# Kernel tuning notes

Hardware: AMD Instinct MI355X
Metric: run time of the kernel (lower is better)

## Reference

```python
import jax, jax.numpy as jnp
import numpy as np

N = 10000      # nodes
E = 65536      # edges
IN = 16        # in_channels
H = 64         # hidden_channels
ED = 4         # edge_attr_dim
MLP_H = 64     # hidden width of edge-weight MLPs


def _glorot(key, shape):
    fan_in, fan_out = shape[0], shape[1]
    lim = np.sqrt(6.0 / (fan_in + fan_out)).astype(np.float32)
    return jax.random.uniform(key, shape, jnp.float32, -lim, lim)


def setup_inputs() -> dict:
    key = jax.random.key(0)
    ks = jax.random.split(key, 16)
    x = jax.random.normal(ks[0], (N, IN), dtype=jnp.float32)
    edge_index = jax.random.randint(ks[1], (2, E), 0, N, dtype=jnp.int64)
    edge_attr = jax.random.normal(ks[2], (E, ED), dtype=jnp.float32)
    return {
        "x": x,
        "edge_index": edge_index,
        "edge_attr": edge_attr,
        # nn1: Linear(ED,64) -> ReLU -> Linear(64, IN*H)
        "nn1_w1": _glorot(ks[3], (ED, MLP_H)), "nn1_b1": jnp.zeros((MLP_H,), jnp.float32),
        "nn1_w2": _glorot(ks[4], (MLP_H, IN * H)), "nn1_b2": jnp.zeros((IN * H,), jnp.float32),
        "root1": _glorot(ks[5], (IN, H)), "bias1": jnp.zeros((H,), jnp.float32),
        # nn2: Linear(ED,64) -> ReLU -> Linear(64, H*H)
        "nn2_w1": _glorot(ks[6], (ED, MLP_H)), "nn2_b1": jnp.zeros((MLP_H,), jnp.float32),
        "nn2_w2": _glorot(ks[7], (MLP_H, H * H)), "nn2_b2": jnp.zeros((H * H,), jnp.float32),
        "root2": _glorot(ks[8], (H, H)), "bias2": jnp.zeros((H,), jnp.float32),
        # readout MLP
        "lin1_w": _glorot(ks[9], (H, 8)), "lin1_b": jnp.zeros((8,), jnp.float32),
        "lin2_w": _glorot(ks[10], (8, 1)), "lin2_b": jnp.zeros((1,), jnp.float32),
    }


def _nnconv(x, src, dst, edge_attr, w1, b1, w2, b2, root, bias, cin, cout):
    # Edge-conditioned weight generation: MLP(edge_attr) -> [E, cin, cout]
    h = jax.nn.relu(edge_attr @ w1 + b1)
    We = (h @ w2 + b2).reshape(-1, cin, cout)
    # Per-edge matmul: message_e = x[src_e] @ We_e  -> [E, cout]
    msg = jnp.einsum('ei,eio->eo', x[src], We)
    # Scatter mean over destination nodes
    s = jax.ops.segment_sum(msg, dst, num_segments=N)
    cnt = jax.ops.segment_sum(jnp.ones((msg.shape[0],), x.dtype), dst, num_segments=N)
    agg = s / jnp.maximum(cnt, 1.0)[:, None]
    # Root transform + bias (PyG NNConv defaults: root_weight=True, bias=True)
    return agg + x @ root + bias


def reference(x, edge_index, edge_attr,
              nn1_w1, nn1_b1, nn1_w2, nn1_b2, root1, bias1,
              nn2_w1, nn2_b1, nn2_w2, nn2_b2, root2, bias2,
              lin1_w, lin1_b, lin2_w, lin2_b):
    # Dropout layers are identity in eval mode.
    src, dst = edge_index[0], edge_index[1]
    h = jax.nn.relu(_nnconv(x, src, dst, edge_attr,
                            nn1_w1, nn1_b1, nn1_w2, nn1_b2, root1, bias1, IN, H))
    h = jax.nn.relu(_nnconv(h, src, dst, edge_attr,
                            nn2_w1, nn2_b1, nn2_w2, nn2_b2, root2, bias2, H, H))
    h = jax.nn.relu(h @ lin1_w + lin1_b)
    return (h @ lin2_w + lin2_b)[:, 0]  # squeeze(-1) -> [N]
```

## Files before the change

### kernel.cpp

```cpp
#include <hip/hip_runtime.h>
#include <hip/hip_bf16.h>

#define NN 10000
#define EE 65536

using short8  = __attribute__((ext_vector_type(8))) short;
using u16x8   = __attribute__((ext_vector_type(8))) unsigned short;
using float4v = __attribute__((ext_vector_type(4))) float;

__device__ __forceinline__ unsigned short f2b(float f){
  union { float f; unsigned int u; } v; v.f = f;
  unsigned int u = v.u;
  unsigned int r = (u + 0x7fff + ((u >> 16) & 1)) >> 16;
  return (unsigned short)r;
}

__device__ __forceinline__ short8 ntload(const unsigned short* p){
  return __builtin_nontemporal_load((const short8*)p);
}



__device__ __forceinline__ void do_permB(int idx, const float* __restrict__ w2,
                                         unsigned short* __restrict__ Bt,
                                         int cin, int s , int cb ){
  int tile   = idx >> 9;
  int within = idx & 511;
  int ot  = tile >> s;
  int k32 = tile & ((1<<s)-1);
  int kk   = within & 31;
  int orow = within >> 5;
  int o = ot*16 + orow;
  int k = k32*32 + kk;
  int m = k >> cb;
  int i = k & (cin-1);
  Bt[idx] = f2b(w2[(size_t)m*(cin*64) + i*64 + o]);
}

__global__ __launch_bounds__(256) void k_prep(
    const float* __restrict__ w2a, unsigned short* __restrict__ Bt1,
    const float* __restrict__ w2b, unsigned short* __restrict__ Bt2,
    int* __restrict__ cnt){
  int b = blockIdx.x;
  int t = threadIdx.x;
  if(b < 40){
    int i = b*256 + t;
    if(i < NN) cnt[i] = 0;
  } else if(b < 296){
    do_permB((b-40)*256 + t, w2a, Bt1, 16, 5, 4);
  } else {
    do_permB((b-296)*256 + t, w2b, Bt2, 64, 7, 6);
  }
}


__global__ void k_hist(const int* __restrict__ dst, int* __restrict__ cnt){
  int e = blockIdx.x*256 + threadIdx.x;
  if(e < EE) atomicAdd(&cnt[dst[e]], 1);
}

__global__ __launch_bounds__(1024) void k_scan(const int* __restrict__ cnt, int* __restrict__ offs, int* __restrict__ cursor){
  const int T = 1024, PER = (NN + T - 1)/T;
  int tid = threadIdx.x;
  int base = tid*PER;
  int local[PER];
  int s = 0;
  #pragma unroll
  for(int j=0;j<PER;j++){
    int i = base+j;
    int v = (i<NN)? cnt[i] : 0;
    local[j] = s;
    s += v;
  }
  int lane = tid & 63, wv = tid >> 6;
  int val = s;
  #pragma unroll
  for(int o=1;o<64;o<<=1){
    int u = __shfl_up(val, o, 64);
    if(lane >= o) val += u;
  }
  __shared__ int wsum[16];
  if(lane==63) wsum[wv] = val;
  __syncthreads();
  if(tid==0){
    int acc=0;
    #pragma unroll
    for(int i=0;i<16;i++){ int t2=wsum[i]; wsum[i]=acc; acc+=t2; }
  }
  __syncthreads();
  int thr_excl = wsum[wv] + (val - s);
  #pragma unroll
  for(int j=0;j<PER;j++){
    int i = base+j;
    if(i<NN){ int e = thr_excl + local[j]; offs[i]=e; cursor[i]=e; }
  }
  if(tid == T-1) offs[NN] = thr_excl + s;
}

__global__ void k_scatter(const int* __restrict__ dst, const int* __restrict__ src,
                          int* __restrict__ cursor, int2* __restrict__ elist2){
  int e = blockIdx.x*256 + threadIdx.x;
  if(e < EE){ int p = atomicAdd(&cursor[dst[e]], 1); elist2[p] = make_int2(e, src[e]); }
}


__global__ __launch_bounds__(64) void k_accK1(const float* __restrict__ x,
    const int* __restrict__ offs, const int2* __restrict__ elist2,
    const float* __restrict__ ea, const float* __restrict__ w1, const float* __restrict__ b1,
    unsigned short* __restrict__ K1, float* __restrict__ XS, int v0){
  int v = v0 + blockIdx.x;
  int L = threadIdx.x;
  int cg = L & 3, mg = L >> 2;
  int i0 = cg << 2;
  float w1c0 = w1[L], w1c1 = w1[64+L], w1c2 = w1[128+L], w1c3 = w1[192+L];
  float b1c = b1[L];
  __shared__ float sh[2][64];
  float acc[4][4];
  #pragma unroll
  for(int j=0;j<4;j++)
    #pragma unroll
    for(int c=0;c<4;c++) acc[j][c]=0.f;
  float4 xs = make_float4(0.f,0.f,0.f,0.f);
  int p0 = offs[v], p1 = offs[v+1];
  float4 a_nxt = make_float4(0.f,0.f,0.f,0.f);
  float4 x_nxt = make_float4(0.f,0.f,0.f,0.f);
  if(p0 < p1){
    int2 es = elist2[p0];
    a_nxt = *(const float4*)(ea + (size_t)es.x*4);
    x_nxt = *(const float4*)(x + (size_t)es.y*16 + i0);
  }
  for(int p=p0;p<p1;p++){
    int buf = (p-p0)&1;
    float4 xv = x_nxt;
    float4 av = a_nxt;
    float hv = fmaxf(b1c + av.x*w1c0 + av.y*w1c1 + av.z*w1c2 + av.w*w1c3, 0.f);
    sh[buf][L] = hv;
    __syncthreads();
    if(p+1<p1){
      int2 es = elist2[p+1];
      a_nxt = *(const float4*)(ea + (size_t)es.x*4);
      x_nxt = *(const float4*)(x + (size_t)es.y*16 + i0);
    }
    xs.x += xv.x; xs.y += xv.y; xs.z += xv.z; xs.w += xv.w;
    #pragma unroll
    for(int j=0;j<4;j++){
      float hm = sh[buf][mg + 16*j];
      acc[j][0] += hm*xv.x; acc[j][1] += hm*xv.y;
      acc[j][2] += hm*xv.z; acc[j][3] += hm*xv.w;
    }
  }
  int r = blockIdx.x;
  int rt = r >> 4, lrow = r & 15;
  #pragma unroll
  for(int j=0;j<4;j++){
    int m = mg + 16*j;
    size_t sidx = ((size_t)(rt*32 + (m>>1)))*512
                + (size_t)lrow*32 + (m&1)*16 + cg*4;
    ushort4 u;
    u.x=f2b(acc[j][0]); u.y=f2b(acc[j][1]); u.z=f2b(acc[j][2]); u.w=f2b(acc[j][3]);
    *(ushort4*)(K1 + sidx) = u;
  }
  if(mg==0) *(float4*)(XS + (size_t)v*64 + i0) = xs;
}


__global__ __launch_bounds__(64) void k_accK2(const float* __restrict__ x1,
    const int* __restrict__ offs, const int2* __restrict__ elist2,
    const float* __restrict__ ea, const float* __restrict__ w1, const float* __restrict__ b1,
    unsigned short* __restrict__ K, float* __restrict__ XS, int v0){
  int v = v0 + blockIdx.x;
  int L = threadIdx.x;
  int cg = L & 7, mg = L >> 3;
  int i0 = cg << 3;
  float w1c0 = w1[L], w1c1 = w1[64+L], w1c2 = w1[128+L], w1c3 = w1[192+L];
  float b1c = b1[L];
  __shared__ float sh[2][64];
  float acc[8][8];
  #pragma unroll
  for(int j=0;j<8;j++)
    #pragma unroll
    for(int c=0;c<8;c++) acc[j][c]=0.f;
  float4 xs0 = make_float4(0.f,0.f,0.f,0.f);
  float4 xs1 = make_float4(0.f,0.f,0.f,0.f);
  int p0 = offs[v], p1 = offs[v+1];
  float4 a_nxt = make_float4(0.f,0.f,0.f,0.f);
  float4 x_nxt0 = make_float4(0.f,0.f,0.f,0.f);
  float4 x_nxt1 = make_float4(0.f,0.f,0.f,0.f);
  if(p0 < p1){
    int2 es = elist2[p0];
    a_nxt = *(const float4*)(ea + (size_t)es.x*4);
    const float* xr = x1 + (size_t)es.y*64 + i0;
    x_nxt0 = *(const float4*)xr;
    x_nxt1 = *(const float4*)(xr+4);
  }
  for(int p=p0;p<p1;p++){
    int buf = (p-p0)&1;
    float4 xv0 = x_nxt0, xv1 = x_nxt1;
    float4 av = a_nxt;
    float hv = fmaxf(b1c + av.x*w1c0 + av.y*w1c1 + av.z*w1c2 + av.w*w1c3, 0.f);
    sh[buf][L] = hv;
    __syncthreads();
    if(p+1<p1){
      int2 es = elist2[p+1];
      a_nxt = *(const float4*)(ea + (size_t)es.x*4);
      const float* xr = x1 + (size_t)es.y*64 + i0;
      x_nxt0 = *(const float4*)xr;
      x_nxt1 = *(const float4*)(xr+4);
    }
    xs0.x += xv0.x; xs0.y += xv0.y; xs0.z += xv0.z; xs0.w += xv0.w;
    xs1.x += xv1.x; xs1.y += xv1.y; xs1.z += xv1.z; xs1.w += xv1.w;
    float4 h4a = *(float4*)&sh[buf][mg*8];
    float4 h4b = *(float4*)&sh[buf][mg*8+4];
    #pragma unroll
    for(int jj=0;jj<2;jj++){
      float4 h4 = jj? h4b : h4a;
      #pragma unroll
      for(int tq=0;tq<4;tq++){
        int j = jj*4+tq;
        float hm = (tq==0)?h4.x:(tq==1)?h4.y:(tq==2)?h4.z:h4.w;
        acc[j][0] += hm*xv0.x; acc[j][1] += hm*xv0.y;
        acc[j][2] += hm*xv0.z; acc[j][3] += hm*xv0.w;
        acc[j][4] += hm*xv1.x; acc[j][5] += hm*xv1.y;
        acc[j][6] += hm*xv1.z; acc[j][7] += hm*xv1.w;
      }
    }
  }
  int r = blockIdx.x;
  int rt = r >> 4, lrow = r & 15;
  #pragma unroll
  for(int j=0;j<8;j++){
    int m = mg*8 + j;
    size_t sidx = ((size_t)(rt*128 + m*2 + (cg>>2)))*512
                + (size_t)lrow*32 + (cg&3)*8;
    u16x8 u;
    #pragma unroll
    for(int c=0;c<8;c++) u[c] = f2b(acc[j][c]);
    *(u16x8*)(K + sidx) = u;
  }
  if(mg==0){
    *(float4*)(XS + (size_t)v*64 + i0)     = xs0;
    *(float4*)(XS + (size_t)v*64 + i0 + 4) = xs1;
  }
}


template<int KT32, int TSTEPS>
__global__ __launch_bounds__(512) void k_gemmS(const unsigned short* __restrict__ A,
    const unsigned short* __restrict__ Bt, float* __restrict__ P,
    int ntiles, int rowsChunk){
  __shared__ unsigned short Bs[4*TSTEPS*512];
  int tid = threadIdx.x;
  int lane = tid & 63;
  int w = tid >> 6;
  int s = blockIdx.y;
  int kbase = s*TSTEPS;

  constexpr int NT = 4*TSTEPS;
  constexpr int PERW = NT/8;
  #pragma unroll
  for(int it=0; it<PERW; it++){
    int g = w*PERW + it;
    int ct = g / TSTEPS, t = g - ct*TSTEPS;
    *(short8*)(Bs + (size_t)g*512 + lane*8) =
        *(const short8*)(Bt + (((size_t)ct*KT32 + kbase + t) << 9) + lane*8);
  }
  __syncthreads();

  int lrt = blockIdx.x*8 + w;
  if(lrt >= ntiles) return;

  int lperm = (lane & 15)*32 + (lane >> 4)*8;
  const unsigned short* Ap = A + (((size_t)lrt*KT32 + kbase) << 9) + lperm;
  const unsigned short* BsL = Bs + lperm;

  float4v acc0{}, acc1{}, acc2{}, acc3{};
  short8 ab[4];
  #pragma unroll
  for(int t=0;t<4;t++) ab[t] = ntload(Ap + t*512);

  #pragma unroll
  for(int t=0;t<TSTEPS;t++){
    short8 a  = ab[t&3];
    short8 b0 = *(const short8*)(BsL + (0*TSTEPS+t)*512);
    short8 b1 = *(const short8*)(BsL + (1*TSTEPS+t)*512);
    short8 b2 = *(const short8*)(BsL + (2*TSTEPS+t)*512);
    short8 b3 = *(const short8*)(BsL + (3*TSTEPS+t)*512);
    acc0 = __builtin_amdgcn_mfma_f32_16x16x32_bf16(a, b0, acc0, 0,0,0);
    acc1 = __builtin_amdgcn_mfma_f32_16x16x32_bf16(a, b1, acc1, 0,0,0);
    acc2 = __builtin_amdgcn_mfma_f32_16x16x32_bf16(a, b2, acc2, 0,0,0);
    acc3 = __builtin_amdgcn_mfma_f32_16x16x32_bf16(a, b3, acc3, 0,0,0);
    if(t+4 < TSTEPS) ab[t&3] = ntload(Ap + (t+4)*512);
  }

  int lrow = lane & 15, quad = lane >> 4;
  float* Pr = P + ((size_t)s*rowsChunk + lrt*16 + quad*4)*64 + lrow;
  #pragma unroll
  for(int reg=0;reg<4;reg++){
    Pr[(size_t)reg*64 +  0] = acc0[reg];
    Pr[(size_t)reg*64 + 16] = acc1[reg];
    Pr[(size_t)reg*64 + 32] = acc2[reg];
    Pr[(size_t)reg*64 + 48] = acc3[reg];
  }
}


template<int CIN, int SPLIT>
__global__ __launch_bounds__(256) void k_reduce_ep(const float* __restrict__ P, int rows, int v0,
    const float* __restrict__ XS, const float* __restrict__ b2, const float* __restrict__ xprev,
    const float* __restrict__ root, const float* __restrict__ bias, const int* __restrict__ offs,
    float* __restrict__ out){
  int idx = blockIdx.x*256 + threadIdx.x;
  if(idx >= rows*16) return;
  int r = idx >> 4, og = (idx & 15) << 2;
  int v = v0 + r;

  float4 s = make_float4(0.f,0.f,0.f,0.f);
  #pragma unroll
  for(int z=0; z<SPLIT; z++){
    float4 p = *(const float4*)(P + ((size_t)z*rows + r)*64 + og);
    s.x += p.x; s.y += p.y; s.z += p.z; s.w += p.w;
  }
  #pragma unroll
  for(int i=0;i<CIN;i++){
    float xsv = XS[(size_t)v*64 + i];
    float4 b = *(const float4*)(b2 + i*64 + og);
    s.x += xsv*b.x; s.y += xsv*b.y; s.z += xsv*b.z; s.w += xsv*b.w;
  }
  float4 rt = make_float4(0.f,0.f,0.f,0.f);
  #pragma unroll
  for(int i=0;i<CIN;i++){
    float xv = xprev[(size_t)v*CIN + i];
    float4 wv = *(const float4*)(root + i*64 + og);
    rt.x += xv*wv.x; rt.y += xv*wv.y; rt.z += xv*wv.z; rt.w += xv*wv.w;
  }
  float c = (float)(offs[v+1]-offs[v]); c = fmaxf(c, 1.f);
  float inv = 1.f/c;
  float4 bi = *(const float4*)(bias + og);
  float4 o;
  o.x = fmaxf(s.x*inv + rt.x + bi.x, 0.f);
  o.y = fmaxf(s.y*inv + rt.y + bi.y, 0.f);
  o.z = fmaxf(s.z*inv + rt.z + bi.z, 0.f);
  o.w = fmaxf(s.w*inv + rt.w + bi.w, 0.f);
  *(float4*)(out + (size_t)v*64 + og) = o;
}


template<int SPLIT>
__global__ __launch_bounds__(256) void k_red2_ro(const float* __restrict__ P, int rows, int v0,
    const float* __restrict__ XS, const float* __restrict__ b2, const float* __restrict__ x1,
    const float* __restrict__ root, const float* __restrict__ bias, const int* __restrict__ offs,
    const float* __restrict__ lw1, const float* __restrict__ lb1,
    const float* __restrict__ lw2, const float* __restrict__ lb2,
    float* __restrict__ out){
  __shared__ float row[16][68];
  __shared__ float hjs[16][8];
  int tid = threadIdx.x;
  int idx = blockIdx.x*256 + tid;
  int r = idx >> 4, og = (idx & 15) << 2;
  int n = tid >> 4;
  int nbase = blockIdx.x*16;
  int ninblk = rows - nbase; if(ninblk > 16) ninblk = 16;

  float4 o = make_float4(0.f,0.f,0.f,0.f);
  if(r < rows){
    int vg = v0 + r;
    float4 s = make_float4(0.f,0.f,0.f,0.f);
    #pragma unroll
    for(int z=0; z<SPLIT; z++){
      float4 p = *(const float4*)(P + ((size_t)z*rows + r)*64 + og);
      s.x += p.x; s.y += p.y; s.z += p.z; s.w += p.w;
    }
    #pragma unroll
    for(int i=0;i<64;i++){
      float xsv = XS[(size_t)vg*64 + i];
      float4 b = *(const float4*)(b2 + i*64 + og);
      s.x += xsv*b.x; s.y += xsv*b.y; s.z += xsv*b.z; s.w += xsv*b.w;
    }
    float4 rt = make_float4(0.f,0.f,0.f,0.f);
    #pragma unroll
    for(int i=0;i<64;i++){
      float xv = x1[(size_t)vg*64 + i];
      float4 wv = *(const float4*)(root + i*64 + og);
      rt.x += xv*wv.x; rt.y += xv*wv.y; rt.z += xv*wv.z; rt.w += xv*wv.w;
    }
    float c = (float)(offs[vg+1]-offs[vg]); c = fmaxf(c, 1.f);
    float inv = 1.f/c;
    float4 bi = *(const float4*)(bias + og);
    o.x = fmaxf(s.x*inv + rt.x + bi.x, 0.f);
    o.y = fmaxf(s.y*inv + rt.y + bi.y, 0.f);
    o.z = fmaxf(s.z*inv + rt.z + bi.z, 0.f);
    o.w = fmaxf(s.w*inv + rt.w + bi.w, 0.f);
  }
  *(float4*)&row[n][og] = o;
  __syncthreads();
  if(tid < 128){
    int n2 = tid >> 3, j = tid & 7;
    if(n2 < ninblk){
      float a = lb1[j];
      #pragma unroll
      for(int i=0;i<64;i++) a += row[n2][i]*lw1[i*8+j];
      hjs[n2][j] = fmaxf(a, 0.f)*lw2[j];
    }
  }
  __syncthreads();
  if(tid < 16 && tid < ninblk){
    float s = lb2[0];
    #pragma unroll
    for(int j=0;j<8;j++) s += hjs[tid][j];
    out[v0 + nbase + tid] = s;
  }
}


extern "C" void kernel_launch(void* const* d_in, const int* in_sizes, int n_in,
                              void* d_out, int out_size, void* d_ws, size_t ws_size,
                              hipStream_t stream) {
  const float* x      = (const float*)d_in[0];
  const int*   ei     = (const int*)d_in[1];
  const float* ea     = (const float*)d_in[2];
  const float* nn1_w1 = (const float*)d_in[3];
  const float* nn1_b1 = (const float*)d_in[4];
  const float* nn1_w2 = (const float*)d_in[5];
  const float* nn1_b2 = (const float*)d_in[6];
  const float* root1  = (const float*)d_in[7];
  const float* bias1  = (const float*)d_in[8];
  const float* nn2_w1 = (const float*)d_in[9];
  const float* nn2_b1 = (const float*)d_in[10];
  const float* nn2_w2 = (const float*)d_in[11];
  const float* nn2_b2 = (const float*)d_in[12];
  const float* root2  = (const float*)d_in[13];
  const float* bias2  = (const float*)d_in[14];
  const float* lin1_w = (const float*)d_in[15];
  const float* lin1_b = (const float*)d_in[16];
  const float* lin2_w = (const float*)d_in[17];
  const float* lin2_b = (const float*)d_in[18];
  float* out = (float*)d_out;

  const int* srcIdx = ei;
  const int* dstIdx = ei + EE;

  char* w = (char*)d_ws;
  size_t off = 0;
  auto alloc = [&](size_t bytes)->void*{
    void* p = w + off;
    off = (off + bytes + 255) & ~(size_t)255;
    return p;
  };
  int*            cnt    = (int*)           alloc((size_t)NN*4);
  int*            offs   = (int*)           alloc((size_t)(NN+1)*4);
  int*            cursor = (int*)           alloc((size_t)NN*4);
  int2*           elist2 = (int2*)          alloc((size_t)EE*8);
  float*          XS     = (float*)         alloc((size_t)NN*64*4);
  float*          x1     = (float*)         alloc((size_t)NN*64*4);
  unsigned short* Bt1    = (unsigned short*)alloc((size_t)64*1024*2);
  unsigned short* Bt2    = (unsigned short*)alloc((size_t)64*4096*2);
  size_t fixedBytes = off;
  size_t R = (ws_size > fixedBytes) ? (ws_size - fixedBytes) : 0;

  const int S1 = 4, S2 = 8;
  size_t needSingle = (size_t)(NN/16)*128*1024 + (size_t)S2*NN*64*4;
  bool single = (R >= needSingle + 4096);

  k_prep   <<<1320, 256, 0, stream>>>(nn1_w2, Bt1, nn2_w2, Bt2, cnt);
  k_hist   <<<(EE+255)/256, 256, 0, stream>>>(dstIdx, cnt);
  k_scan   <<<1, 1024, 0, stream>>>(cnt, offs, cursor);
  k_scatter<<<(EE+255)/256, 256, 0, stream>>>(dstIdx, srcIdx, cursor, elist2);

  if(single){
    unsigned short* Kbuf = (unsigned short*)(w + off);
    float* P = (float*)(w + off + (size_t)(NN/16)*128*1024);
    int ntiles = NN/16;
    int gx = (ntiles + 7)/8;

    k_accK1 <<<NN, 64, 0, stream>>>(x, offs, elist2, ea, nn1_w1, nn1_b1, Kbuf, XS, 0);
    k_gemmS<32,8> <<<dim3(gx, S1), 512, 0, stream>>>(Kbuf, Bt1, P, ntiles, NN);
    k_reduce_ep<16,S1><<<(NN*16+255)/256, 256, 0, stream>>>(P, NN, 0, XS, nn1_b2, x,
                                                             root1, bias1, offs, x1);
    k_accK2 <<<NN, 64, 0, stream>>>(x1, offs, elist2, ea, nn2_w1, nn2_b1, Kbuf, XS, 0);
    k_gemmS<128,16><<<dim3(gx, S2), 512, 0, stream>>>(Kbuf, Bt2, P, ntiles, NN);
    k_red2_ro<S2><<<(NN+15)/16, 256, 0, stream>>>(P, NN, 0, XS, nn2_b2, x1, root2, bias2, offs,
                                                   lin1_w, lin1_b, lin2_w, lin2_b, out);
  } else {
    long long C2 = (long long)(R / (8192 + S2*256));
    long long C1 = (long long)(R / (2048 + S1*256));
    if(C2 > NN) C2 = NN; if(C1 > NN) C1 = NN;
    C2 &= ~127LL; C1 &= ~127LL;
    if(C2 < 128) C2 = 128; if(C1 < 128) C1 = 128;
    unsigned short* Kbuf = (unsigned short*)(w + off);
    {
      float* P = (float*)(w + off + (size_t)C1*2048);
      for(long long v0=0; v0<NN; v0+=C1){
        int rows = (int)((NN - v0 < C1) ? (NN - v0) : C1);
        int nt = rows/16, gx = (nt + 7)/8;
        k_accK1<<<rows, 64, 0, stream>>>(x, offs, elist2, ea, nn1_w1, nn1_b1, Kbuf, XS, (int)v0);
        k_gemmS<32,8><<<dim3(gx, S1), 512, 0, stream>>>(Kbuf, Bt1, P, nt, rows);
        k_reduce_ep<16,S1><<<(rows*16+255)/256, 256, 0, stream>>>(P, rows, (int)v0, XS, nn1_b2, x,
                                                                   root1, bias1, offs, x1);
      }
    }
    {
      float* P = (float*)(w + off + (size_t)C2*8192);
      for(long long v0=0; v0<NN; v0+=C2){
        int rows = (int)((NN - v0 < C2) ? (NN - v0) : C2);
        int nt = rows/16, gx = (nt + 7)/8;
        k_accK2<<<rows, 64, 0, stream>>>(x1, offs, elist2, ea, nn2_w1, nn2_b1, Kbuf, XS, (int)v0);
        k_gemmS<128,16><<<dim3(gx, S2), 512, 0, stream>>>(Kbuf, Bt2, P, nt, rows);
        k_red2_ro<S2><<<(rows+15)/16, 256, 0, stream>>>(P, rows, (int)v0, XS, nn2_b2, x1,
                                                         root2, bias2, offs,
                                                         lin1_w, lin1_b, lin2_w, lin2_b, out);
      }
    }
  }
}
```

Measured before the change: 206.5 us.

## Fuse layer-1 GEMM with reduce epilogue, dropping split-K partials

Layer 1 replaces the split-K GEMM (4 slices writing partials) and the separate reduce/epilogue kernel with one kernel. Each wave does the full K=1024 reduction over a 128 KB LDS copy of B, then applies the bias-term, root transform, mean and ReLU directly from the accumulators. This removes a kernel launch and the partial-sum round trip through memory. In exchange there is less grid parallelism (one slice instead of four), lower occupancy from the large LDS use, and strided scalar loads in the epilogue.

```diff
diff --git a/kernel.cpp b/kernel.cpp
--- a/kernel.cpp
+++ b/kernel.cpp
@@ -244,6 +244,85 @@
 }
 
 
+__global__ __launch_bounds__(512) void k_gemmS1F(const unsigned short* __restrict__ A,
+    const unsigned short* __restrict__ Bt,
+    const float* __restrict__ XS, const float* __restrict__ eb,
+    const float* __restrict__ xp, const float* __restrict__ rw,
+    const float* __restrict__ bw, const int* __restrict__ offs,
+    float* __restrict__ x1out, int ntiles, int v0){
+  __shared__ unsigned short Bs[65536];
+  int tid = threadIdx.x;
+  int lane = tid & 63;
+  int w = tid >> 6;
+
+  #pragma unroll
+  for(int it=0; it<16; it++)
+    *(short8*)(Bs + it*4096 + tid*8) = *(const short8*)(Bt + it*4096 + tid*8);
+  __syncthreads();
+
+  int lrt = blockIdx.x*8 + w;
+  if(lrt >= ntiles) return;
+
+  int lperm = (lane & 15)*32 + (lane >> 4)*8;
+  const unsigned short* Ap = A + (((size_t)lrt*32) << 9) + lperm;
+  const unsigned short* BsL = Bs + lperm;
+
+  float4v acc0{}, acc1{}, acc2{}, acc3{};
+  short8 ab[4];
+  #pragma unroll
+  for(int t=0;t<4;t++) ab[t] = ntload(Ap + t*512);
+
+  #pragma unroll
+  for(int t=0;t<32;t++){
+    short8 a  = ab[t&3];
+    short8 b0 = *(const short8*)(BsL + (0*32+t)*512);
+    short8 b1 = *(const short8*)(BsL + (1*32+t)*512);
+    short8 b2 = *(const short8*)(BsL + (2*32+t)*512);
+    short8 b3 = *(const short8*)(BsL + (3*32+t)*512);
+    acc0 = __builtin_amdgcn_mfma_f32_16x16x32_bf16(a, b0, acc0, 0,0,0);
+    acc1 = __builtin_amdgcn_mfma_f32_16x16x32_bf16(a, b1, acc1, 0,0,0);
+    acc2 = __builtin_amdgcn_mfma_f32_16x16x32_bf16(a, b2, acc2, 0,0,0);
+    acc3 = __builtin_amdgcn_mfma_f32_16x16x32_bf16(a, b3, acc3, 0,0,0);
+    if(t+4 < 32) ab[t&3] = ntload(Ap + (t+4)*512);
+  }
+
+  int lrow = lane & 15, quad = lane >> 4;
+  int vb = v0 + lrt*16 + quad*4;
+  float s[4][4], tt[4][4];
+  #pragma unroll
+  for(int reg=0; reg<4; reg++){
+    s[reg][0]=acc0[reg]; s[reg][1]=acc1[reg]; s[reg][2]=acc2[reg]; s[reg][3]=acc3[reg];
+    tt[reg][0]=0.f; tt[reg][1]=0.f; tt[reg][2]=0.f; tt[reg][3]=0.f;
+  }
+  #pragma unroll 4
+  for(int i=0;i<16;i++){
+    float e0 = eb[i*64 +  0 + lrow], e1 = eb[i*64 + 16 + lrow];
+    float e2 = eb[i*64 + 32 + lrow], e3 = eb[i*64 + 48 + lrow];
+    float r0 = rw[i*64 +  0 + lrow], r1 = rw[i*64 + 16 + lrow];
+    float r2 = rw[i*64 + 32 + lrow], r3 = rw[i*64 + 48 + lrow];
+    #pragma unroll
+    for(int reg=0; reg<4; reg++){
+      float xsv = XS[(size_t)(vb+reg)*64 + i];
+      float xpv = xp[(size_t)(vb+reg)*16 + i];
+      s[reg][0] += xsv*e0; s[reg][1] += xsv*e1; s[reg][2] += xsv*e2; s[reg][3] += xsv*e3;
+      tt[reg][0] += xpv*r0; tt[reg][1] += xpv*r1; tt[reg][2] += xpv*r2; tt[reg][3] += xpv*r3;
+    }
+  }
+  float bw0 = bw[lrow], bw1 = bw[16+lrow], bw2 = bw[32+lrow], bw3 = bw[48+lrow];
+  #pragma unroll
+  for(int reg=0; reg<4; reg++){
+    int v = vb + reg;
+    float dg = fmaxf((float)(offs[v+1]-offs[v]), 1.f);
+    float inv = 1.f/dg;
+    float* xr = x1out + (size_t)v*64 + lrow;
+    xr[ 0] = fmaxf(s[reg][0]*inv + tt[reg][0] + bw0, 0.f);
+    xr[16] = fmaxf(s[reg][1]*inv + tt[reg][1] + bw1, 0.f);
+    xr[32] = fmaxf(s[reg][2]*inv + tt[reg][2] + bw2, 0.f);
+    xr[48] = fmaxf(s[reg][3]*inv + tt[reg][3] + bw3, 0.f);
+  }
+}
+
+
 template<int KT32, int TSTEPS>
 __global__ __launch_bounds__(512) void k_gemmS(const unsigned short* __restrict__ A,
     const unsigned short* __restrict__ Bt, float* __restrict__ P,
@@ -301,47 +380,6 @@
     Pr[(size_t)reg*64 + 32] = acc2[reg];
     Pr[(size_t)reg*64 + 48] = acc3[reg];
   }
-}
-
-
-template<int CIN, int SPLIT>
-__global__ __launch_bounds__(256) void k_reduce_ep(const float* __restrict__ P, int rows, int v0,
-    const float* __restrict__ XS, const float* __restrict__ b2, const float* __restrict__ xprev,
-    const float* __restrict__ root, const float* __restrict__ bias, const int* __restrict__ offs,
-    float* __restrict__ out){
-  int idx = blockIdx.x*256 + threadIdx.x;
-  if(idx >= rows*16) return;
-  int r = idx >> 4, og = (idx & 15) << 2;
-  int v = v0 + r;
-
-  float4 s = make_float4(0.f,0.f,0.f,0.f);
-  #pragma unroll
-  for(int z=0; z<SPLIT; z++){
-    float4 p = *(const float4*)(P + ((size_t)z*rows + r)*64 + og);
-    s.x += p.x; s.y += p.y; s.z += p.z; s.w += p.w;
-  }
-  #pragma unroll
-  for(int i=0;i<CIN;i++){
-    float xsv = XS[(size_t)v*64 + i];
-    float4 b = *(const float4*)(b2 + i*64 + og);
-    s.x += xsv*b.x; s.y += xsv*b.y; s.z += xsv*b.z; s.w += xsv*b.w;
-  }
-  float4 rt = make_float4(0.f,0.f,0.f,0.f);
-  #pragma unroll
-  for(int i=0;i<CIN;i++){
-    float xv = xprev[(size_t)v*CIN + i];
-    float4 wv = *(const float4*)(root + i*64 + og);
-    rt.x += xv*wv.x; rt.y += xv*wv.y; rt.z += xv*wv.z; rt.w += xv*wv.w;
-  }
-  float c = (float)(offs[v+1]-offs[v]); c = fmaxf(c, 1.f);
-  float inv = 1.f/c;
-  float4 bi = *(const float4*)(bias + og);
-  float4 o;
-  o.x = fmaxf(s.x*inv + rt.x + bi.x, 0.f);
-  o.y = fmaxf(s.y*inv + rt.y + bi.y, 0.f);
-  o.z = fmaxf(s.z*inv + rt.z + bi.z, 0.f);
-  o.w = fmaxf(s.w*inv + rt.w + bi.w, 0.f);
-  *(float4*)(out + (size_t)v*64 + og) = o;
 }
 
 
@@ -457,7 +495,7 @@
   size_t fixedBytes = off;
   size_t R = (ws_size > fixedBytes) ? (ws_size - fixedBytes) : 0;
 
-  const int S1 = 4, S2 = 8;
+  const int S2 = 8;
   size_t needSingle = (size_t)(NN/16)*128*1024 + (size_t)S2*NN*64*4;
   bool single = (R >= needSingle + 4096);
 
@@ -473,29 +511,26 @@
     int gx = (ntiles + 7)/8;
 
     k_accK1 <<<NN, 64, 0, stream>>>(x, offs, elist2, ea, nn1_w1, nn1_b1, Kbuf, XS, 0);
-    k_gemmS<32,8> <<<dim3(gx, S1), 512, 0, stream>>>(Kbuf, Bt1, P, ntiles, NN);
-    k_reduce_ep<16,S1><<<(NN*16+255)/256, 256, 0, stream>>>(P, NN, 0, XS, nn1_b2, x,
-                                                             root1, bias1, offs, x1);
+    k_gemmS1F<<<gx, 512, 0, stream>>>(Kbuf, Bt1, XS, nn1_b2, x, root1, bias1, offs,
+                                      x1, ntiles, 0);
     k_accK2 <<<NN, 64, 0, stream>>>(x1, offs, elist2, ea, nn2_w1, nn2_b1, Kbuf, XS, 0);
     k_gemmS<128,16><<<dim3(gx, S2), 512, 0, stream>>>(Kbuf, Bt2, P, ntiles, NN);
     k_red2_ro<S2><<<(NN+15)/16, 256, 0, stream>>>(P, NN, 0, XS, nn2_b2, x1, root2, bias2, offs,
                                                    lin1_w, lin1_b, lin2_w, lin2_b, out);
   } else {
     long long C2 = (long long)(R / (8192 + S2*256));
-    long long C1 = (long long)(R / (2048 + S1*256));
+    long long C1 = (long long)(R / 2048);
     if(C2 > NN) C2 = NN; if(C1 > NN) C1 = NN;
     C2 &= ~127LL; C1 &= ~127LL;
     if(C2 < 128) C2 = 128; if(C1 < 128) C1 = 128;
     unsigned short* Kbuf = (unsigned short*)(w + off);
     {
-      float* P = (float*)(w + off + (size_t)C1*2048);
       for(long long v0=0; v0<NN; v0+=C1){
         int rows = (int)((NN - v0 < C1) ? (NN - v0) : C1);
         int nt = rows/16, gx = (nt + 7)/8;
         k_accK1<<<rows, 64, 0, stream>>>(x, offs, elist2, ea, nn1_w1, nn1_b1, Kbuf, XS, (int)v0);
-        k_gemmS<32,8><<<dim3(gx, S1), 512, 0, stream>>>(Kbuf, Bt1, P, nt, rows);
-        k_reduce_ep<16,S1><<<(rows*16+255)/256, 256, 0, stream>>>(P, rows, (int)v0, XS, nn1_b2, x,
-                                                                   root1, bias1, offs, x1);
+        k_gemmS1F<<<gx, 512, 0, stream>>>(Kbuf, Bt1, XS, nn1_b2, x, root1, bias1, offs,
+                                          x1, nt, (int)v0);
       }
     }
     {
```

Result: no change. 206.7 us (+0.1%).
